# Performance work log

Hardware: AMD Instinct MI355X
Metric: run time of the kernel (lower is better)

## Reference

```python
import jax, jax.numpy as jnp
import numpy as np

EMBED, MID = 2048, 256
SLOPE = 0.2

def _lrelu(v):
    return jnp.where(v >= 0, v, SLOPE * v)

def setup_inputs() -> dict:
    key = jax.random.key(0)
    ks = jax.random.split(key, 9)
    B, C, L = 4, EMBED, 4096
    s_in = 1.0 / np.sqrt(C)
    s_mid = 1.0 / np.sqrt(MID)
    return {
        "x":   jax.random.normal(ks[0], (B, C, L), dtype=jnp.float32),
        "W_t": jax.random.uniform(ks[1], (MID, C), jnp.float32, -s_in, s_in),
        "b_t": jax.random.uniform(ks[2], (MID,), jnp.float32, -s_in, s_in),
        "W_p": jax.random.uniform(ks[3], (MID, C), jnp.float32, -s_in, s_in),
        "b_p": jax.random.uniform(ks[4], (MID,), jnp.float32, -s_in, s_in),
        "W_g": jax.random.uniform(ks[5], (MID, C), jnp.float32, -s_in, s_in),
        "b_g": jax.random.uniform(ks[6], (MID,), jnp.float32, -s_in, s_in),
        "W_o": jax.random.uniform(ks[7], (C, MID), jnp.float32, -s_mid, s_mid),
        "b_o": jax.random.uniform(ks[8], (C,), jnp.float32, -s_mid, s_mid),
    }

def reference(x, W_t, b_t, W_p, b_p, W_g, b_g, W_o, b_o):
    # x: [B, C, L]; 1x1 conv == channel matmul. Dropout is identity (eval mode).
    theta = _lrelu(jnp.einsum('mc,bcl->bml', W_t, x) + b_t[None, :, None])  # [B, M, L]
    phi   = _lrelu(jnp.einsum('mc,bcl->bml', W_p, x) + b_p[None, :, None])  # [B, M, L]
    gamma = _lrelu(jnp.einsum('mc,bcl->bml', W_g, x) + b_g[None, :, None])  # [B, M, L]
    # scores: phi^T @ theta -> [B, L, L], fixed scale 1/32
    scores = jnp.einsum('bmi,bmj->bij', phi, theta) / 32.0
    attn = jax.nn.softmax(scores, axis=-1)
    # y: attn @ gamma^T -> [B, L, M], then back to [B, M, L]
    y = jnp.einsum('bij,bmj->bmi', attn, gamma)
    out = x + _lrelu(jnp.einsum('cm,bml->bcl', W_o, y) + b_o[None, :, None])
    return out
```

## Files before the change

kernel.cpp:

```cpp
#include <hip/hip_runtime.h>
#include <stdint.h>

#define B_ 4
#define C_ 2048
#define L_ 4096
#define M_ 256
#define M3_ 768
#define SLOPE_ 0.2f
#define SPLIT_ 4
#define KVB_ 32

typedef __attribute__((ext_vector_type(8))) short short8;
typedef __attribute__((ext_vector_type(4))) float f32x4;

__device__ __forceinline__ unsigned short f2bf(float f) {
    union { float f; unsigned u; } v; v.f = f;
    unsigned r = v.u + 0x7FFF + ((v.u >> 16) & 1);
    return (unsigned short)(r >> 16);
}
__device__ __forceinline__ unsigned short f2bf_rz(float f) {
    union { float f; unsigned u; } v; v.f = f;
    return (unsigned short)(v.u >> 16);
}
__device__ __forceinline__ unsigned pack2(float a, float b) {
    return (unsigned)f2bf(a) | ((unsigned)f2bf(b) << 16);
}
__device__ __forceinline__ float bf2f(unsigned short u) {
    union { unsigned u; float f; } v; v.u = (unsigned)u << 16; return v.f;
}
__device__ __forceinline__ float lrelu(float v) { return v >= 0.f ? v : SLOPE_ * v; }

__device__ __forceinline__ void gload_lds16(const void* g, void* l) {
    __builtin_amdgcn_global_load_lds(
        (const __attribute__((address_space(1))) void*)g,
        (__attribute__((address_space(3))) void*)l, 16, 0, 0);
}

__global__ __launch_bounds__(256) void prep_x(
    const float* __restrict__ x, unsigned short* __restrict__ xT)
{
    const int l = blockIdx.x * 64 + (threadIdx.x & 63);
    const int c = blockIdx.y * 32 + (threadIdx.x >> 6) * 8;
    const int b = blockIdx.z;
    const float* src = x + ((size_t)b * C_ + c) * L_ + l;
    unsigned v[4];
    #pragma unroll
    for (int j = 0; j < 4; ++j)
        v[j] = pack2(src[(size_t)(2 * j) * L_], src[(size_t)(2 * j + 1) * L_]);
    *reinterpret_cast<uint4*>(&xT[((size_t)b * L_ + l) * C_ + c]) =
        *reinterpret_cast<uint4*>(v);
}

__global__ __launch_bounds__(256) void prep_w(
    const float* __restrict__ Wt, const float* __restrict__ Wp,
    const float* __restrict__ Wg, const float* __restrict__ Wo,
    unsigned short* __restrict__ w3, unsigned short* __restrict__ wo)
{
    const size_t NW = (size_t)M_ * C_;
    size_t e = ((size_t)blockIdx.x * 256 + threadIdx.x) * 8;
    const float* src; unsigned short* dst;
    if (e < NW)          { src = Wt + e;          dst = w3 + e; }
    else if (e < 2 * NW) { src = Wp + (e - NW);   dst = w3 + e; }
    else if (e < 3 * NW) { src = Wg + (e - 2*NW); dst = w3 + e; }
    else                 { src = Wo + (e - 3*NW); dst = wo + (e - 3*NW); }
    float4 a = *reinterpret_cast<const float4*>(src);
    float4 b = *reinterpret_cast<const float4*>(src + 4);
    unsigned v[4] = { pack2(a.x, a.y), pack2(a.z, a.w),
                      pack2(b.x, b.y), pack2(b.z, b.w) };
    *reinterpret_cast<uint4*>(dst) = *reinterpret_cast<uint4*>(v);
}

__global__ __launch_bounds__(256, 3) void proj_kernel(
    const unsigned short* __restrict__ w3,
    const float* __restrict__ bt, const float* __restrict__ bp,
    const float* __restrict__ bg,
    const unsigned short* __restrict__ xT,
    unsigned short* __restrict__ theta,
    unsigned short* __restrict__ phi,
    unsigned short* __restrict__ gammaT)
{
    __shared__ unsigned short As[128 * 64];
    __shared__ unsigned short Bs[128 * 64];

    const int l0 = blockIdx.x * 128;
    const int m0 = blockIdx.y * 128;
    const int b  = blockIdx.z;
    const int t  = threadIdx.x;
    const int wave = t >> 6, lane = t & 63;
    const int lr = lane & 15, lg = lane >> 4;
    const int wm = (wave >> 1) * 64, wl = (wave & 1) * 64;

    const int which = m0 >> 8;
    const float* bsrc = (which == 0) ? bt : (which == 1) ? bp : bg;
    const int mw = m0 & 255;

    const unsigned short* abase = w3 + (size_t)m0 * C_;
    const unsigned short* bbase = xT + ((size_t)b * L_ + l0) * C_;

    const int srow = lane >> 3;
    const int scol = ((lane & 7) ^ srow) * 8;

    f32x4 acc[4][4] = {};

    for (int k0 = 0; k0 < C_; k0 += 64) {
        __syncthreads();
        #pragma unroll
        for (int i = 0; i < 4; ++i) {
            int chunk = wave * 4 + i;
            int row = chunk * 8 + srow;
            gload_lds16(abase + (size_t)row * C_ + k0 + scol, As + chunk * 512);
            gload_lds16(bbase + (size_t)row * C_ + k0 + scol, Bs + chunk * 512);
        }
        __syncthreads();

        #pragma unroll
        for (int ks = 0; ks < 2; ++ks) {
            short8 af[4], bf[4];
            #pragma unroll
            for (int mi = 0; mi < 4; ++mi)
                af[mi] = *reinterpret_cast<const short8*>(
                    &As[(wm + mi * 16 + lr) * 64 +
                        ((ks * 32 + lg * 8) ^ ((lr & 7) << 3))]);
            #pragma unroll
            for (int ni = 0; ni < 4; ++ni)
                bf[ni] = *reinterpret_cast<const short8*>(
                    &Bs[(wl + ni * 16 + lr) * 64 +
                        ((ks * 32 + lg * 8) ^ ((lr & 7) << 3))]);
            #pragma unroll
            for (int mi = 0; mi < 4; ++mi)
                #pragma unroll
                for (int ni = 0; ni < 4; ++ni)
                    acc[mi][ni] = __builtin_amdgcn_mfma_f32_16x16x32_bf16(
                        af[mi], bf[ni], acc[mi][ni], 0, 0, 0);
        }
    }

    if (which < 2) {
        unsigned short* dst = (which == 0) ? theta : phi;
        const float scale = (which == 1) ? 0.03125f : 1.0f;
        #pragma unroll
        for (int mi = 0; mi < 4; ++mi) {
            const int mloc = mw + wm + mi * 16 + lg * 4;
            float b0 = bsrc[mloc], b1 = bsrc[mloc + 1];
            float b2 = bsrc[mloc + 2], b3 = bsrc[mloc + 3];
            #pragma unroll
            for (int ni = 0; ni < 4; ++ni) {
                int l = l0 + wl + ni * 16 + lr;
                uint2 pk;
                pk.x = pack2(lrelu(acc[mi][ni][0] + b0) * scale,
                             lrelu(acc[mi][ni][1] + b1) * scale);
                pk.y = pack2(lrelu(acc[mi][ni][2] + b2) * scale,
                             lrelu(acc[mi][ni][3] + b3) * scale);
                *reinterpret_cast<uint2*>(&dst[((size_t)b * L_ + l) * M_ + mloc]) = pk;
            }
        }
    } else {
        #pragma unroll
        for (int mi = 0; mi < 4; ++mi) {
            #pragma unroll
            for (int r = 0; r < 4; ++r) {
                int m = mw + wm + mi * 16 + lg * 4 + r;
                float bias = bsrc[m];
                #pragma unroll
                for (int ni = 0; ni < 4; ++ni) {
                    int l = l0 + wl + ni * 16 + lr;
                    gammaT[((size_t)b * M_ + m) * L_ + l] =
                        f2bf(lrelu(acc[mi][ni][r] + bias));
                }
            }
        }
    }
}

__global__ __launch_bounds__(512, 1) void attn_kernel(
    const unsigned short* __restrict__ phi,
    const unsigned short* __restrict__ theta,
    const unsigned short* __restrict__ gammaT,
    unsigned short* __restrict__ yp,
    float* __restrict__ rsp)
{
    __shared__ unsigned short Ks[2][KVB_ * 256];
    __shared__ unsigned short Vs[2][256 * KVB_];
    __shared__ unsigned short Ps[8][32][42];

    const int q0 = blockIdx.x * 256;
    const int s  = blockIdx.y;
    const int b  = blockIdx.z;
    const int kvbase = s * (L_ / SPLIT_);
    const int t  = threadIdx.x;
    const int wave = t >> 6, lane = t & 63;
    const int lr = lane & 15, lg = lane >> 4;

    const unsigned short* theta_b = theta  + (size_t)b * L_ * M_;
    const unsigned short* gamma_b = gammaT + (size_t)b * M_ * L_;

    short8 qf[2][8];
    #pragma unroll
    for (int u = 0; u < 2; ++u) {
        const unsigned short* qrow =
            phi + ((size_t)b * L_ + q0 + wave * 32 + u * 16 + lr) * M_ + lg * 8;
        #pragma unroll
        for (int ks = 0; ks < 8; ++ks)
            qf[u][ks] = *reinterpret_cast<const short8*>(qrow + ks * 32);
    }

    f32x4 accy[2][16] = {};
    float rsum[2][4] = {};

    auto stage_k = [&](unsigned short* buf, int kv0) {
        #pragma unroll
        for (int q = 0; q < 2; ++q) {
            int c   = q * 512 + t;
            int row = c >> 5;
            int cb  = (c & 31) << 4;
            int cbs = cb ^ ((row & 7) << 4);
            const unsigned short* src = theta_b + (size_t)(kv0 + row) * M_ + (cbs >> 1);
            unsigned short* ldst = buf + ((size_t)(q * 512 + wave * 64) << 3);
            gload_lds16(src, ldst);
        }
    };
    auto stage_v = [&](unsigned short* buf, int kv0) {
        #pragma unroll
        for (int q = 0; q < 2; ++q) {
            int c  = q * 512 + t;
            int mh = c >> 3;
            int tb = ((c & 7) << 4) ^ ((mh & 7) << 4);
            int m  = mh * 2 + (tb >> 6);
            int j  = (tb & 63) >> 1;
            const unsigned short* src = gamma_b + (size_t)m * L_ + kv0 + j;
            unsigned short* ldst = buf + ((size_t)(q * 512 + wave * 64) << 3);
            gload_lds16(src, ldst);
        }
    };

    stage_k(&Ks[0][0], kvbase);
    stage_v(&Vs[0][0], kvbase);
    __syncthreads();

    int cur = 0;
    for (int it = 0; it < L_ / SPLIT_ / KVB_; ++it) {
        if (it + 1 < L_ / SPLIT_ / KVB_) {
            stage_k(&Ks[cur ^ 1][0], kvbase + (it + 1) * KVB_);
            stage_v(&Vs[cur ^ 1][0], kvbase + (it + 1) * KVB_);
        }

        f32x4 sacc[2][2] = {};
        __builtin_amdgcn_s_setprio(1);
        #pragma unroll
        for (int ks = 0; ks < 8; ++ks) {
            #pragma unroll
            for (int jt = 0; jt < 2; ++jt) {
                int jr = jt * 16 + lr;
                int cbl = ks * 64 + lg * 16;
                short8 bf = *reinterpret_cast<const short8*>(
                    &Ks[cur][jr * 256 + (((cbl ^ ((jr & 7) << 4)) >> 1))]);
                sacc[0][jt] = __builtin_amdgcn_mfma_f32_16x16x32_bf16(qf[0][ks], bf, sacc[0][jt], 0, 0, 0);
                sacc[1][jt] = __builtin_amdgcn_mfma_f32_16x16x32_bf16(qf[1][ks], bf, sacc[1][jt], 0, 0, 0);
            }
        }
        __builtin_amdgcn_s_setprio(0);

        #pragma unroll
        for (int u = 0; u < 2; ++u)
            #pragma unroll
            for (int jt = 0; jt < 2; ++jt)
                #pragma unroll
                for (int r = 0; r < 4; ++r) {
                    float p = __expf(sacc[u][jt][r]);
                    rsum[u][r] += p;
                    Ps[wave][u * 16 + lg * 4 + r][lr + 16 * jt] = f2bf_rz(p);
                }

        short8 paf[2];
        paf[0] = *reinterpret_cast<const short8*>(&Ps[wave][lr][lg * 8]);
        paf[1] = *reinterpret_cast<const short8*>(&Ps[wave][16 + lr][lg * 8]);
        __builtin_amdgcn_s_setprio(1);
        #pragma unroll
        for (int mt = 0; mt < 16; ++mt) {
            int m = mt * 16 + lr;
            int byte = (m >> 1) * 128 +
                       ((((m & 1) * 64 + lg * 16)) ^ (((m >> 1) & 7) << 4));
            short8 bf = *reinterpret_cast<const short8*>(&Vs[cur][byte >> 1]);
            accy[0][mt] = __builtin_amdgcn_mfma_f32_16x16x32_bf16(paf[0], bf, accy[0][mt], 0, 0, 0);
            accy[1][mt] = __builtin_amdgcn_mfma_f32_16x16x32_bf16(paf[1], bf, accy[1][mt], 0, 0, 0);
        }
        __builtin_amdgcn_s_setprio(0);

        __syncthreads();
        cur ^= 1;
    }

    unsigned short* ypb = yp + (((size_t)(s * B_ + b) * L_) + q0) * M_;
    #pragma unroll
    for (int u = 0; u < 2; ++u)
        #pragma unroll
        for (int r = 0; r < 4; ++r) {
            int row = wave * 32 + u * 16 + lg * 4 + r;
            #pragma unroll
            for (int mt = 0; mt < 16; ++mt)
                ypb[(size_t)row * M_ + lr + 16 * mt] = f2bf(accy[u][mt][r]);
            float ssum = rsum[u][r];
            #pragma unroll
            for (int off = 1; off < 16; off <<= 1)
                ssum += __shfl_xor(ssum, off, 64);
            if (lr == 0)
                rsp[((size_t)(s * B_ + b) * L_) + q0 + row] = ssum;
        }
}

__global__ __launch_bounds__(256) void reduce_kernel(
    const unsigned short* __restrict__ yp,
    const float* __restrict__ rsp,
    unsigned short* __restrict__ y)
{
    const int idx = blockIdx.x * 256 + threadIdx.x;
    const int ml  = (idx * 8) & (M_ - 1);
    const int row = (idx * 8) >> 8;
    const int b   = row >> 12;
    const int l   = row & (L_ - 1);

    float acc[8] = {};
    float rs = 0.f;
    #pragma unroll
    for (int s = 0; s < SPLIT_; ++s) {
        uint4 raw = *reinterpret_cast<const uint4*>(
            &yp[(((size_t)(s * B_ + b) * L_) + l) * M_ + ml]);
        const unsigned* dw = reinterpret_cast<const unsigned*>(&raw);
        #pragma unroll
        for (int k = 0; k < 4; ++k) {
            acc[2 * k]     += bf2f((unsigned short)(dw[k] & 0xFFFF));
            acc[2 * k + 1] += bf2f((unsigned short)(dw[k] >> 16));
        }
        rs += rsp[((size_t)(s * B_ + b) * L_) + l];
    }
    float inv = 1.f / rs;
    unsigned v[4] = { pack2(acc[0] * inv, acc[1] * inv),
                      pack2(acc[2] * inv, acc[3] * inv),
                      pack2(acc[4] * inv, acc[5] * inv),
                      pack2(acc[6] * inv, acc[7] * inv) };
    *reinterpret_cast<uint4*>(&y[((size_t)b * L_ + l) * M_ + ml]) =
        *reinterpret_cast<uint4*>(v);
}

__global__ __launch_bounds__(256, 3) void out_kernel(
    const float* __restrict__ x,
    const unsigned short* __restrict__ wo,
    const float* __restrict__ bo,
    const unsigned short* __restrict__ y,
    float* __restrict__ out)
{
    __shared__ unsigned short As[128 * 64];
    __shared__ unsigned short Bs[128 * 64];

    const int l0 = blockIdx.x * 128;
    const int c0 = blockIdx.y * 128;
    const int b  = blockIdx.z;
    const int t  = threadIdx.x;
    const int wave = t >> 6, lane = t & 63;
    const int lr = lane & 15, lg = lane >> 4;
    const int wm = (wave >> 1) * 64, wl = (wave & 1) * 64;

    const unsigned short* abase = wo + (size_t)c0 * M_;
    const unsigned short* bbase = y + ((size_t)b * L_ + l0) * M_;

    const int srow = lane >> 3;
    const int scol = ((lane & 7) ^ srow) * 8;

    f32x4 acc[4][4] = {};

    for (int k0 = 0; k0 < M_; k0 += 64) {
        __syncthreads();
        #pragma unroll
        for (int i = 0; i < 4; ++i) {
            int chunk = wave * 4 + i;
            int row = chunk * 8 + srow;
            gload_lds16(abase + (size_t)row * M_ + k0 + scol, As + chunk * 512);
            gload_lds16(bbase + (size_t)row * M_ + k0 + scol, Bs + chunk * 512);
        }
        __syncthreads();

        #pragma unroll
        for (int ks = 0; ks < 2; ++ks) {
            short8 af[4], bf[4];
            #pragma unroll
            for (int mi = 0; mi < 4; ++mi)
                af[mi] = *reinterpret_cast<const short8*>(
                    &As[(wm + mi * 16 + lr) * 64 +
                        ((ks * 32 + lg * 8) ^ ((lr & 7) << 3))]);
            #pragma unroll
            for (int ni = 0; ni < 4; ++ni)
                bf[ni] = *reinterpret_cast<const short8*>(
                    &Bs[(wl + ni * 16 + lr) * 64 +
                        ((ks * 32 + lg * 8) ^ ((lr & 7) << 3))]);
            #pragma unroll
            for (int mi = 0; mi < 4; ++mi)
                #pragma unroll
                for (int ni = 0; ni < 4; ++ni)
                    acc[mi][ni] = __builtin_amdgcn_mfma_f32_16x16x32_bf16(
                        af[mi], bf[ni], acc[mi][ni], 0, 0, 0);
        }
    }

    #pragma unroll
    for (int mi = 0; mi < 4; ++mi) {
        #pragma unroll
        for (int r = 0; r < 4; ++r) {
            int c = c0 + wm + mi * 16 + lg * 4 + r;
            float bias = bo[c];
            #pragma unroll
            for (int ni = 0; ni < 4; ++ni) {
                int l = l0 + wl + ni * 16 + lr;
                size_t idx = ((size_t)b * C_ + c) * L_ + l;
                out[idx] = x[idx] + lrelu(acc[mi][ni][r] + bias);
            }
        }
    }
}

extern "C" void kernel_launch(void* const* d_in, const int* in_sizes, int n_in,
                              void* d_out, int out_size, void* d_ws, size_t ws_size,
                              hipStream_t stream) {
    const float* x  = (const float*)d_in[0];
    const float* Wt = (const float*)d_in[1];
    const float* bt = (const float*)d_in[2];
    const float* Wp = (const float*)d_in[3];
    const float* bp = (const float*)d_in[4];
    const float* Wg = (const float*)d_in[5];
    const float* bg = (const float*)d_in[6];
    const float* Wo = (const float*)d_in[7];
    const float* bo = (const float*)d_in[8];
    float* out = (float*)d_out;

    unsigned short* xT    = (unsigned short*)d_ws;
    unsigned short* w3    = xT + (size_t)B_ * L_ * C_;
    unsigned short* wob   = w3 + (size_t)M3_ * C_;
    unsigned short* theta = wob + (size_t)C_ * M_;
    unsigned short* phi   = theta + (size_t)B_ * L_ * M_;
    unsigned short* gammaT= phi   + (size_t)B_ * L_ * M_;

    unsigned short* yp = xT;
    float* rsp = (float*)w3;
    unsigned short* yb = theta;

    prep_x<<<dim3(L_ / 64, C_ / 32, B_), 256, 0, stream>>>(x, xT);
    prep_w<<<dim3(2097152 / 8 / 256), 256, 0, stream>>>(Wt, Wp, Wg, Wo, w3, wob);
    proj_kernel<<<dim3(L_ / 128, M3_ / 128, B_), 256, 0, stream>>>(
        w3, bt, bp, bg, xT, theta, phi, gammaT);
    attn_kernel<<<dim3(L_ / 256, SPLIT_, B_), 512, 0, stream>>>(
        phi, theta, gammaT, yp, rsp);
    reduce_kernel<<<dim3((B_ * L_ * M_ / 8) / 256), 256, 0, stream>>>(yp, rsp, yb);
    out_kernel<<<dim3(L_ / 128, C_ / 128, B_), 256, 0, stream>>>(x, wob, bo, yb, out);
}
```

Before: 263.9 us.

## Switch attention to 32x32x16 MFMA with register-only P transpose

Reworks the attention kernel to use 32x32x16 bf16 MFMAs, computing S transposed (K as A operand, Q as B) so each lane holds exp scores for one query column. P is packed to bf16 and redistributed across lanes with permlane32_swap instead of going through an LDS scratch buffer, removing the Ps shared array, its writes and reads, and the 16-lane shuffle reduction of row sums. The V staging swizzle and the output write mapping are changed to match the new fragment layout. It risks layout or swizzle mismatches and a different register footprint for the larger accumulators.

```diff
diff --git a/kernel.cpp b/kernel.cpp
--- a/kernel.cpp
+++ b/kernel.cpp
@@ -12,15 +12,16 @@
 
 typedef __attribute__((ext_vector_type(8))) short short8;
 typedef __attribute__((ext_vector_type(4))) float f32x4;
+typedef __attribute__((ext_vector_type(16))) float f32x16;
+typedef __attribute__((ext_vector_type(2))) int int2v;
 
 __device__ __forceinline__ unsigned short f2bf(float f) {
     union { float f; unsigned u; } v; v.f = f;
     unsigned r = v.u + 0x7FFF + ((v.u >> 16) & 1);
     return (unsigned short)(r >> 16);
 }
-__device__ __forceinline__ unsigned short f2bf_rz(float f) {
-    union { float f; unsigned u; } v; v.f = f;
-    return (unsigned short)(v.u >> 16);
+__device__ __forceinline__ unsigned fbits(float f) {
+    union { float f; unsigned u; } v; v.f = f; return v.u;
 }
 __device__ __forceinline__ unsigned pack2(float a, float b) {
     return (unsigned)f2bf(a) | ((unsigned)f2bf(b) << 16);
@@ -181,7 +182,6 @@
 {
     __shared__ unsigned short Ks[2][KVB_ * 256];
     __shared__ unsigned short Vs[2][256 * KVB_];
-    __shared__ unsigned short Ps[8][32][42];
 
     const int q0 = blockIdx.x * 256;
     const int s  = blockIdx.y;
@@ -189,23 +189,22 @@
     const int kvbase = s * (L_ / SPLIT_);
     const int t  = threadIdx.x;
     const int wave = t >> 6, lane = t & 63;
-    const int lr = lane & 15, lg = lane >> 4;
+    const int l31 = lane & 31, h = lane >> 5;
 
     const unsigned short* theta_b = theta  + (size_t)b * L_ * M_;
     const unsigned short* gamma_b = gammaT + (size_t)b * M_ * L_;
 
-    short8 qf[2][8];
-    #pragma unroll
-    for (int u = 0; u < 2; ++u) {
+    short8 qf[16];
+    {
         const unsigned short* qrow =
-            phi + ((size_t)b * L_ + q0 + wave * 32 + u * 16 + lr) * M_ + lg * 8;
-        #pragma unroll
-        for (int ks = 0; ks < 8; ++ks)
-            qf[u][ks] = *reinterpret_cast<const short8*>(qrow + ks * 32);
-    }
-
-    f32x4 accy[2][16] = {};
-    float rsum[2][4] = {};
+            phi + ((size_t)b * L_ + q0 + wave * 32 + l31) * M_ + h * 8;
+        #pragma unroll
+        for (int st = 0; st < 16; ++st)
+            qf[st] = *reinterpret_cast<const short8*>(qrow + st * 16);
+    }
+
+    f32x16 accy[8] = {};
+    float rsum = 0.f;
 
     auto stage_k = [&](unsigned short* buf, int kv0) {
         #pragma unroll
@@ -222,12 +221,10 @@
     auto stage_v = [&](unsigned short* buf, int kv0) {
         #pragma unroll
         for (int q = 0; q < 2; ++q) {
-            int c  = q * 512 + t;
-            int mh = c >> 3;
-            int tb = ((c & 7) << 4) ^ ((mh & 7) << 4);
-            int m  = mh * 2 + (tb >> 6);
-            int j  = (tb & 63) >> 1;
-            const unsigned short* src = gamma_b + (size_t)m * L_ + kv0 + j;
+            int c   = q * 512 + t;
+            int m   = c >> 2;
+            int k16 = (c & 3) ^ ((m >> 1) & 3);
+            const unsigned short* src = gamma_b + (size_t)m * L_ + kv0 + k16 * 8;
             unsigned short* ldst = buf + ((size_t)(q * 512 + wave * 64) << 3);
             gload_lds16(src, ldst);
         }
@@ -236,6 +233,9 @@
     stage_k(&Ks[0][0], kvbase);
     stage_v(&Vs[0][0], kvbase);
     __syncthreads();
+
+    const int kxk = l31 & 7;
+    const int kxv = (l31 >> 1) & 3;
 
     int cur = 0;
     for (int it = 0; it < L_ / SPLIT_ / KVB_; ++it) {
@@ -244,45 +244,46 @@
             stage_v(&Vs[cur ^ 1][0], kvbase + (it + 1) * KVB_);
         }
 
-        f32x4 sacc[2][2] = {};
+        f32x16 sacc = {};
         __builtin_amdgcn_s_setprio(1);
         #pragma unroll
-        for (int ks = 0; ks < 8; ++ks) {
-            #pragma unroll
-            for (int jt = 0; jt < 2; ++jt) {
-                int jr = jt * 16 + lr;
-                int cbl = ks * 64 + lg * 16;
-                short8 bf = *reinterpret_cast<const short8*>(
-                    &Ks[cur][jr * 256 + (((cbl ^ ((jr & 7) << 4)) >> 1))]);
-                sacc[0][jt] = __builtin_amdgcn_mfma_f32_16x16x32_bf16(qf[0][ks], bf, sacc[0][jt], 0, 0, 0);
-                sacc[1][jt] = __builtin_amdgcn_mfma_f32_16x16x32_bf16(qf[1][ks], bf, sacc[1][jt], 0, 0, 0);
+        for (int st = 0; st < 16; ++st) {
+            short8 kf = *reinterpret_cast<const short8*>(
+                &Ks[cur][l31 * 256 + (((st * 2 + h) ^ kxk) << 3)]);
+            sacc = __builtin_amdgcn_mfma_f32_32x32x16_bf16(kf, qf[st], sacc, 0, 0, 0);
+        }
+        __builtin_amdgcn_s_setprio(0);
+
+        unsigned d[8];
+        #pragma unroll
+        for (int i = 0; i < 8; ++i) {
+            float p0 = __expf(sacc[2 * i]);
+            float p1 = __expf(sacc[2 * i + 1]);
+            rsum += p0 + p1;
+            d[i] = __builtin_amdgcn_perm(fbits(p1), fbits(p0), 0x07060302u);
+        }
+        short8 paf[2];
+        #pragma unroll
+        for (int s2 = 0; s2 < 2; ++s2) {
+            int2v r0 = __builtin_amdgcn_permlane32_swap(
+                (int)d[4 * s2], (int)d[4 * s2 + 2], false, false);
+            int2v r1 = __builtin_amdgcn_permlane32_swap(
+                (int)d[4 * s2 + 1], (int)d[4 * s2 + 3], false, false);
+            unsigned w[4] = { (unsigned)r0.x, (unsigned)r1.x,
+                              (unsigned)r0.y, (unsigned)r1.y };
+            paf[s2] = *reinterpret_cast<short8*>(w);
+        }
+
+        __builtin_amdgcn_s_setprio(1);
+        #pragma unroll
+        for (int mt = 0; mt < 8; ++mt) {
+            #pragma unroll
+            for (int s2 = 0; s2 < 2; ++s2) {
+                short8 vf = *reinterpret_cast<const short8*>(
+                    &Vs[cur][(mt * 32 + l31) * 32 + (((s2 * 2 + h) ^ kxv) << 3)]);
+                accy[mt] = __builtin_amdgcn_mfma_f32_32x32x16_bf16(
+                    paf[s2], vf, accy[mt], 0, 0, 0);
             }
-        }
-        __builtin_amdgcn_s_setprio(0);
-
-        #pragma unroll
-        for (int u = 0; u < 2; ++u)
-            #pragma unroll
-            for (int jt = 0; jt < 2; ++jt)
-                #pragma unroll
-                for (int r = 0; r < 4; ++r) {
-                    float p = __expf(sacc[u][jt][r]);
-                    rsum[u][r] += p;
-                    Ps[wave][u * 16 + lg * 4 + r][lr + 16 * jt] = f2bf_rz(p);
-                }
-
-        short8 paf[2];
-        paf[0] = *reinterpret_cast<const short8*>(&Ps[wave][lr][lg * 8]);
-        paf[1] = *reinterpret_cast<const short8*>(&Ps[wave][16 + lr][lg * 8]);
-        __builtin_amdgcn_s_setprio(1);
-        #pragma unroll
-        for (int mt = 0; mt < 16; ++mt) {
-            int m = mt * 16 + lr;
-            int byte = (m >> 1) * 128 +
-                       ((((m & 1) * 64 + lg * 16)) ^ (((m >> 1) & 7) << 4));
-            short8 bf = *reinterpret_cast<const short8*>(&Vs[cur][byte >> 1]);
-            accy[0][mt] = __builtin_amdgcn_mfma_f32_16x16x32_bf16(paf[0], bf, accy[0][mt], 0, 0, 0);
-            accy[1][mt] = __builtin_amdgcn_mfma_f32_16x16x32_bf16(paf[1], bf, accy[1][mt], 0, 0, 0);
         }
         __builtin_amdgcn_s_setprio(0);
 
@@ -291,21 +292,17 @@
     }
 
     unsigned short* ypb = yp + (((size_t)(s * B_ + b) * L_) + q0) * M_;
+    float tot = rsum + __shfl_xor(rsum, 32, 64);
+    if (h == 0)
+        rsp[((size_t)(s * B_ + b) * L_) + q0 + wave * 32 + l31] = tot;
     #pragma unroll
-    for (int u = 0; u < 2; ++u)
-        #pragma unroll
-        for (int r = 0; r < 4; ++r) {
-            int row = wave * 32 + u * 16 + lg * 4 + r;
-            #pragma unroll
-            for (int mt = 0; mt < 16; ++mt)
-                ypb[(size_t)row * M_ + lr + 16 * mt] = f2bf(accy[u][mt][r]);
-            float ssum = rsum[u][r];
-            #pragma unroll
-            for (int off = 1; off < 16; off <<= 1)
-                ssum += __shfl_xor(ssum, off, 64);
-            if (lr == 0)
-                rsp[((size_t)(s * B_ + b) * L_) + q0 + row] = ssum;
-        }
+    for (int mt = 0; mt < 8; ++mt) {
+        #pragma unroll
+        for (int r = 0; r < 16; ++r) {
+            int q = wave * 32 + (r & 3) + 8 * (r >> 2) + 4 * h;
+            ypb[(size_t)q * M_ + mt * 32 + l31] = f2bf(accy[mt][r]);
+        }
+    }
 }
 
 __global__ __launch_bounds__(256) void reduce_kernel(
```

After: 256.3 us. 2.9% less time.
